# Kernel tuning notes

Hardware: AMD Instinct MI355X
Metric: run time of the kernel (lower is better)

Reference implementation:

```python
import jax, jax.numpy as jnp
import numpy as np


def overlap_and_add(frames, step):
    # frames: [B, F, L] -> [B, (F-1)*step + L] via strided scatter-add
    B, F, L = frames.shape
    out_len = (F - 1) * step + L
    idx = (jnp.arange(F)[:, None] * step + jnp.arange(L)[None, :]).reshape(-1)  # [F*L]
    return jnp.zeros((B, out_len), frames.dtype).at[:, idx].add(frames.reshape(B, F * L))


def setup_inputs() -> dict:
    key = jax.random.key(0)
    k1, k2, k3 = jax.random.split(key, 3)
    bs, frame, basis, spk = 16, 4086, 512, 2
    L = 16  # kernel_size_enc
    speech_length = (frame - 1) * (L // 2) + L  # 32696
    inputs = jax.random.normal(k1, (bs, frame, basis), dtype=jnp.float32)
    estmask = jax.random.uniform(k2, (bs, frame, basis, spk), dtype=jnp.float32)
    W = jax.random.normal(k3, (basis, L), dtype=jnp.float32) * 0.05
    return {"inputs": inputs, "estmask": estmask, "W": W,
            "kernel_size_enc": L, "speech_length": speech_length}


def reference(inputs, estmask, W, kernel_size_enc, speech_length):
    bs, frame, basis = inputs.shape
    spk = estmask.shape[-1]
    # mask-weight: [bs, frame, basis, spk]
    x = inputs[..., None] * estmask
    # -> [bs*spk, frame, basis]
    x = jnp.transpose(x, (0, 3, 1, 2)).reshape(bs * spk, frame, basis)
    # dense projection (no bias, no activation): [bs*spk, frame, L]
    x = jnp.einsum('bfc,cl->bfl', x, W)
    # overlap-and-add with frame_step = L // 2
    x = overlap_and_add(x, kernel_size_enc // 2)  # [bs*spk, samples]
    return x.reshape(bs, spk, speech_length)
```

## Files before the change

### kernel.cpp

```cpp
#include <hip/hip_runtime.h>

constexpr int BS = 16, F = 4086, C = 512, SPK = 2, L = 16, STEP = 8;
constexpr int T    = (F - 1) * STEP + L;
constexpr int ROWS = BS * F;
constexpr int OUT_N = BS * SPK * T;
constexpr int WPAD = 20;
constexpr int WAVES = 4;
constexpr int BLOCK = WAVES * 64;
constexpr int FR  = 4;
constexpr int FPB = WAVES * FR;
constexpr int GRID_A = ROWS / FPB;

template <int CTRL>
__device__ __forceinline__ float dppq(float x) {
    int i = __builtin_bit_cast(int, x);
    i = __builtin_amdgcn_update_dpp(i, i, CTRL, 0xf, 0xf, true);
    return __builtin_bit_cast(float, i);
}
template <int OFF>
__device__ __forceinline__ float swz(float x) {
    int i = __builtin_bit_cast(int, x);
    i = __builtin_amdgcn_ds_swizzle(i, OFF);
    return __builtin_bit_cast(float, i);
}

__device__ __forceinline__ float fold32(float v[32], int lane) {
    const bool h1 = lane & 1, h2 = lane & 2, h4 = lane & 4, h8 = lane & 8, h16 = lane & 16;
#pragma unroll
    for (int i = 0; i < 16; ++i) {
        const float s = h1 ? v[i] : v[i + 16];
        const float k = h1 ? v[i + 16] : v[i];
        v[i] = k + dppq<0xB1>(s);
    }
#pragma unroll
    for (int i = 0; i < 8; ++i) {
        const float s = h2 ? v[i] : v[i + 8];
        const float k = h2 ? v[i + 8] : v[i];
        v[i] = k + dppq<0x4E>(s);
    }
#pragma unroll
    for (int i = 0; i < 4; ++i) {
        const float s = h4 ? v[i] : v[i + 4];
        const float k = h4 ? v[i + 4] : v[i];
        v[i] = k + swz<0x101F>(s);
    }
#pragma unroll
    for (int i = 0; i < 2; ++i) {
        const float s = h8 ? v[i] : v[i + 2];
        const float k = h8 ? v[i + 2] : v[i];
        v[i] = k + swz<0x201F>(s);
    }
    {
        const float s = h16 ? v[0] : v[1];
        const float k = h16 ? v[1] : v[0];
        v[0] = k + swz<0x401F>(s);
    }
    return v[0] + __shfl_xor(v[0], 32, 64);
}

template <bool USE_WS>
__global__ __launch_bounds__(BLOCK, 2) void decoder_proj_kernel(
    const float* __restrict__ inp,
    const float* __restrict__ mask,
    const float* __restrict__ W,
    float* __restrict__ dst)
{
    __shared__ float w_lds[C * WPAD];

    const int tid = threadIdx.x;
    for (int r = tid; r < C; r += BLOCK) {
        const float4* src = reinterpret_cast<const float4*>(W + r * L);
        float4* d = reinterpret_cast<float4*>(w_lds + r * WPAD);
        d[0] = src[0]; d[1] = src[1]; d[2] = src[2]; d[3] = src[3];
    }
    __syncthreads();

    const int wave = tid >> 6, lane = tid & 63;
    const int row0 = blockIdx.x * FPB + wave * FR;

    const int o = ((lane & 1) << 4) | (((lane >> 1) & 1) << 3) | (((lane >> 2) & 1) << 2)
                | (((lane >> 3) & 1) << 1) | ((lane >> 4) & 1);

    float  xiA[8], xiB[8];
    float2 xmA[8], xmB[8];

    auto load = [&](int row, float* xi, float2* xm) {
        const float*  ir = inp + (size_t)row * C;
        const float2* mr = reinterpret_cast<const float2*>(mask) + (size_t)row * C;
#pragma unroll
        for (int i = 0; i < 8; ++i) {
            const int c = lane + 64 * i;
            xi[i] = ir[c];
            xm[i] = mr[c];
        }
    };

    auto compute = [&](const float* xi, const float2* xm) -> float {
        float v[32];
#pragma unroll
        for (int j = 0; j < 32; ++j) v[j] = 0.f;
#pragma unroll
        for (int i = 0; i < 8; ++i) {
            const int c  = lane + 64 * i;
            const float p0 = xi[i] * xm[i].x;
            const float p1 = xi[i] * xm[i].y;
            const float4* wr = reinterpret_cast<const float4*>(&w_lds[c * WPAD]);
#pragma unroll
            for (int q = 0; q < 4; ++q) {
                const float4 wv = wr[q];
                v[4*q+0]    = fmaf(p0, wv.x, v[4*q+0]);
                v[4*q+1]    = fmaf(p0, wv.y, v[4*q+1]);
                v[4*q+2]    = fmaf(p0, wv.z, v[4*q+2]);
                v[4*q+3]    = fmaf(p0, wv.w, v[4*q+3]);
                v[16+4*q+0] = fmaf(p1, wv.x, v[16+4*q+0]);
                v[16+4*q+1] = fmaf(p1, wv.y, v[16+4*q+1]);
                v[16+4*q+2] = fmaf(p1, wv.z, v[16+4*q+2]);
                v[16+4*q+3] = fmaf(p1, wv.w, v[16+4*q+3]);
            }
        }
        return fold32(v, lane);
    };

    auto store = [&](int row, float val) {
        if (USE_WS) {
            if (lane < 32) dst[(size_t)row * 32 + o] = val;
        } else {
            if (lane < 32) {
                const int b = row / F, f = row % F;
                const int s = o >> 4, l = o & 15;
                atomicAdd(&dst[(size_t)(b * SPK + s) * T + f * STEP + l], val);
            }
        }
    };

    load(row0 + 0, xiA, xmA);
    load(row0 + 1, xiB, xmB);
    store(row0 + 0, compute(xiA, xmA));
    load(row0 + 2, xiA, xmA);
    store(row0 + 1, compute(xiB, xmB));
    load(row0 + 3, xiB, xmB);
    store(row0 + 2, compute(xiA, xmA));
    store(row0 + 3, compute(xiB, xmB));
}

__global__ __launch_bounds__(256) void overlap_add_kernel(
    const float* __restrict__ proj,
    float* __restrict__ out)
{
    const int idx = blockIdx.x * blockDim.x + threadIdx.x;
    if (idx >= OUT_N) return;
    const int b = idx / (SPK * T);
    const int r = idx - b * (SPK * T);
    const int s = r / T;
    const int t = r - s * T;
    const int f0 = t >> 3, l0 = t & 7;
    float acc = 0.f;
    if (t < F * STEP) acc += proj[(size_t)(b * F + f0) * 32 + s * 16 + l0];
    if (t >= STEP)    acc += proj[(size_t)(b * F + f0 - 1) * 32 + s * 16 + 8 + l0];
    out[idx] = acc;
}

extern "C" void kernel_launch(void* const* d_in, const int* in_sizes, int n_in,
                              void* d_out, int out_size, void* d_ws, size_t ws_size,
                              hipStream_t stream) {
    const float* inp  = (const float*)d_in[0];
    const float* mask = (const float*)d_in[1];
    const float* W    = (const float*)d_in[2];
    float* out = (float*)d_out;

    const size_t need = (size_t)ROWS * 32 * sizeof(float);
    if (ws_size >= need) {
        float* proj = (float*)d_ws;
        decoder_proj_kernel<true><<<GRID_A, BLOCK, 0, stream>>>(inp, mask, W, proj);
        overlap_add_kernel<<<(OUT_N + 255) / 256, 256, 0, stream>>>(proj, out);
    } else {
        hipMemsetAsync(out, 0, (size_t)OUT_N * sizeof(float), stream);
        decoder_proj_kernel<false><<<GRID_A, BLOCK, 0, stream>>>(inp, mask, W, out);
    }
}
```

Before: 86.42 us.

## Store W transposed as packed bf16 in LDS and vectorize row loads

The projection weights are now converted to bf16 and stored transposed and packed in LDS, which cuts LDS footprint from about 40KB to 16KB and allows four blocks per CU. Input and mask rows are loaded as contiguous float4 vectors per lane instead of strided scalar and float2 loads, and the inner loop reads 8 packed weights per LDS access. The fallback path without workspace is removed. The bf16 rounding of W changes numerical precision, and the code now assumes the workspace is always large enough.

Result: slower. 94.18 us (+9.0%).

```diff
diff --git a/kernel.cpp b/kernel.cpp
--- a/kernel.cpp
+++ b/kernel.cpp
@@ -4,7 +4,6 @@
 constexpr int T    = (F - 1) * STEP + L;
 constexpr int ROWS = BS * F;
 constexpr int OUT_N = BS * SPK * T;
-constexpr int WPAD = 20;
 constexpr int WAVES = 4;
 constexpr int BLOCK = WAVES * 64;
 constexpr int FR  = 4;
@@ -58,20 +57,38 @@
     return v[0] + __shfl_xor(v[0], 32, 64);
 }
 
-template <bool USE_WS>
-__global__ __launch_bounds__(BLOCK, 2) void decoder_proj_kernel(
+__device__ __forceinline__ unsigned short f32_to_bf16_rne(float f) {
+    unsigned int u = __builtin_bit_cast(unsigned int, f);
+    u += 0x7fffu + ((u >> 16) & 1u);
+    return (unsigned short)(u >> 16);
+}
+
+__global__ __launch_bounds__(BLOCK, 4) void decoder_proj_kernel(
     const float* __restrict__ inp,
     const float* __restrict__ mask,
     const float* __restrict__ W,
     float* __restrict__ dst)
 {
-    __shared__ float w_lds[C * WPAD];
+    __shared__ unsigned int wT[L * (C / 2)];
 
     const int tid = threadIdx.x;
-    for (int r = tid; r < C; r += BLOCK) {
-        const float4* src = reinterpret_cast<const float4*>(W + r * L);
-        float4* d = reinterpret_cast<float4*>(w_lds + r * WPAD);
-        d[0] = src[0]; d[1] = src[1]; d[2] = src[2]; d[3] = src[3];
+
+    {
+        const float4* r0 = reinterpret_cast<const float4*>(W + (2 * tid) * L);
+        const float4* r1 = reinterpret_cast<const float4*>(W + (2 * tid + 1) * L);
+        float a[L], b[L];
+#pragma unroll
+        for (int q = 0; q < 4; ++q) {
+            const float4 x = r0[q], y = r1[q];
+            a[4*q+0]=x.x; a[4*q+1]=x.y; a[4*q+2]=x.z; a[4*q+3]=x.w;
+            b[4*q+0]=y.x; b[4*q+1]=y.y; b[4*q+2]=y.z; b[4*q+3]=y.w;
+        }
+#pragma unroll
+        for (int l = 0; l < L; ++l) {
+            const unsigned int d = (unsigned int)f32_to_bf16_rne(a[l])
+                                 | ((unsigned int)f32_to_bf16_rne(b[l]) << 16);
+            wT[l * (C / 2) + tid] = d;
+        }
     }
     __syncthreads();
 
@@ -81,66 +98,66 @@
     const int o = ((lane & 1) << 4) | (((lane >> 1) & 1) << 3) | (((lane >> 2) & 1) << 2)
                 | (((lane >> 3) & 1) << 1) | ((lane >> 4) & 1);
 
-    float  xiA[8], xiB[8];
-    float2 xmA[8], xmB[8];
+    float4 iA0, iA1, mA0, mA1, mA2, mA3;
+    float4 iB0, iB1, mB0, mB1, mB2, mB3;
 
-    auto load = [&](int row, float* xi, float2* xm) {
-        const float*  ir = inp + (size_t)row * C;
-        const float2* mr = reinterpret_cast<const float2*>(mask) + (size_t)row * C;
-#pragma unroll
-        for (int i = 0; i < 8; ++i) {
-            const int c = lane + 64 * i;
-            xi[i] = ir[c];
-            xm[i] = mr[c];
-        }
+    auto load = [&](int row, float4& i0, float4& i1,
+                    float4& m0, float4& m1, float4& m2, float4& m3) {
+        const float4* ir = reinterpret_cast<const float4*>(inp + (size_t)row * C + 8 * lane);
+        const float4* mr = reinterpret_cast<const float4*>(mask + (size_t)row * C * SPK + 16 * lane);
+        i0 = ir[0]; i1 = ir[1];
+        m0 = mr[0]; m1 = mr[1]; m2 = mr[2]; m3 = mr[3];
     };
 
-    auto compute = [&](const float* xi, const float2* xm) -> float {
+    const int4* wT4 = reinterpret_cast<const int4*>(wT);
+
+    auto compute = [&](const float4& i0, const float4& i1,
+                       const float4& m0, const float4& m1,
+                       const float4& m2, const float4& m3) -> float {
+        float p0[8], p1[8];
+        p0[0]=i0.x*m0.x; p1[0]=i0.x*m0.y;  p0[1]=i0.y*m0.z; p1[1]=i0.y*m0.w;
+        p0[2]=i0.z*m1.x; p1[2]=i0.z*m1.y;  p0[3]=i0.w*m1.z; p1[3]=i0.w*m1.w;
+        p0[4]=i1.x*m2.x; p1[4]=i1.x*m2.y;  p0[5]=i1.y*m2.z; p1[5]=i1.y*m2.w;
+        p0[6]=i1.z*m3.x; p1[6]=i1.z*m3.y;  p0[7]=i1.w*m3.z; p1[7]=i1.w*m3.w;
+
         float v[32];
 #pragma unroll
         for (int j = 0; j < 32; ++j) v[j] = 0.f;
+
 #pragma unroll
-        for (int i = 0; i < 8; ++i) {
-            const int c  = lane + 64 * i;
-            const float p0 = xi[i] * xm[i].x;
-            const float p1 = xi[i] * xm[i].y;
-            const float4* wr = reinterpret_cast<const float4*>(&w_lds[c * WPAD]);
+        for (int l = 0; l < L; ++l) {
+            const int4 wd = wT4[l * (C / 8) + lane];
+            const int d0 = wd.x, d1 = wd.y, d2 = wd.z, d3 = wd.w;
+            float w[8];
+            w[0] = __builtin_bit_cast(float, d0 << 16);
+            w[1] = __builtin_bit_cast(float, d0 & 0xffff0000);
+            w[2] = __builtin_bit_cast(float, d1 << 16);
+            w[3] = __builtin_bit_cast(float, d1 & 0xffff0000);
+            w[4] = __builtin_bit_cast(float, d2 << 16);
+            w[5] = __builtin_bit_cast(float, d2 & 0xffff0000);
+            w[6] = __builtin_bit_cast(float, d3 << 16);
+            w[7] = __builtin_bit_cast(float, d3 & 0xffff0000);
 #pragma unroll
-            for (int q = 0; q < 4; ++q) {
-                const float4 wv = wr[q];
-                v[4*q+0]    = fmaf(p0, wv.x, v[4*q+0]);
-                v[4*q+1]    = fmaf(p0, wv.y, v[4*q+1]);
-                v[4*q+2]    = fmaf(p0, wv.z, v[4*q+2]);
-                v[4*q+3]    = fmaf(p0, wv.w, v[4*q+3]);
-                v[16+4*q+0] = fmaf(p1, wv.x, v[16+4*q+0]);
-                v[16+4*q+1] = fmaf(p1, wv.y, v[16+4*q+1]);
-                v[16+4*q+2] = fmaf(p1, wv.z, v[16+4*q+2]);
-                v[16+4*q+3] = fmaf(p1, wv.w, v[16+4*q+3]);
+            for (int k = 0; k < 8; ++k) {
+                v[l]      = fmaf(p0[k], w[k], v[l]);
+                v[16 + l] = fmaf(p1[k], w[k], v[16 + l]);
             }
         }
         return fold32(v, lane);
     };
 
     auto store = [&](int row, float val) {
-        if (USE_WS) {
-            if (lane < 32) dst[(size_t)row * 32 + o] = val;
-        } else {
-            if (lane < 32) {
-                const int b = row / F, f = row % F;
-                const int s = o >> 4, l = o & 15;
-                atomicAdd(&dst[(size_t)(b * SPK + s) * T + f * STEP + l], val);
-            }
-        }
+        if (lane < 32) dst[(size_t)row * 32 + o] = val;
     };
 
-    load(row0 + 0, xiA, xmA);
-    load(row0 + 1, xiB, xmB);
-    store(row0 + 0, compute(xiA, xmA));
-    load(row0 + 2, xiA, xmA);
-    store(row0 + 1, compute(xiB, xmB));
-    load(row0 + 3, xiB, xmB);
-    store(row0 + 2, compute(xiA, xmA));
-    store(row0 + 3, compute(xiB, xmB));
+    load(row0 + 0, iA0, iA1, mA0, mA1, mA2, mA3);
+    load(row0 + 1, iB0, iB1, mB0, mB1, mB2, mB3);
+    store(row0 + 0, compute(iA0, iA1, mA0, mA1, mA2, mA3));
+    load(row0 + 2, iA0, iA1, mA0, mA1, mA2, mA3);
+    store(row0 + 1, compute(iB0, iB1, mB0, mB1, mB2, mB3));
+    load(row0 + 3, iB0, iB1, mB0, mB1, mB2, mB3);
+    store(row0 + 2, compute(iA0, iA1, mA0, mA1, mA2, mA3));
+    store(row0 + 3, compute(iB0, iB1, mB0, mB1, mB2, mB3));
 }
 
 __global__ __launch_bounds__(256) void overlap_add_kernel(
@@ -168,13 +185,7 @@
     const float* W    = (const float*)d_in[2];
     float* out = (float*)d_out;
 
-    const size_t need = (size_t)ROWS * 32 * sizeof(float);
-    if (ws_size >= need) {
-        float* proj = (float*)d_ws;
-        decoder_proj_kernel<true><<<GRID_A, BLOCK, 0, stream>>>(inp, mask, W, proj);
-        overlap_add_kernel<<<(OUT_N + 255) / 256, 256, 0, stream>>>(proj, out);
-    } else {
-        hipMemsetAsync(out, 0, (size_t)OUT_N * sizeof(float), stream);
-        decoder_proj_kernel<false><<<GRID_A, BLOCK, 0, stream>>>(inp, mask, W, out);
-    }
+    float* proj = (float*)d_ws;
+    decoder_proj_kernel<<<GRID_A, BLOCK, 0, stream>>>(inp, mask, W, proj);
+    overlap_add_kernel<<<(OUT_N + 255) / 256, 256, 0, stream>>>(proj, out);
 }
```

## Hold W as packed fp16 in registers and use fdot2 with split-channel wave pairs

Applied to the files above, without the earlier changes.

The projection kernel stops staging W in shared memory. Each lane now holds fp16-packed weights for four fixed channels in registers, and the masked products are converted to fp16 so each FMA pair becomes one v_dot2 instruction. Channels are split across pairs of waves, each wave handling 8 frames, and the partial sums are combined through a small LDS buffer. Input and mask are read with wider float4 loads. This removes LDS weight traffic and cuts ALU work, but it lowers precision to fp16 inputs with fp32 accumulation and drops the fallback path for when no workspace is available.

Result: slower. 99.45 us (+15.1%).

```diff
diff --git a/kernel.cpp b/kernel.cpp
--- a/kernel.cpp
+++ b/kernel.cpp
@@ -4,12 +4,13 @@
 constexpr int T    = (F - 1) * STEP + L;
 constexpr int ROWS = BS * F;
 constexpr int OUT_N = BS * SPK * T;
-constexpr int WPAD = 20;
-constexpr int WAVES = 4;
-constexpr int BLOCK = WAVES * 64;
-constexpr int FR  = 4;
-constexpr int FPB = WAVES * FR;
-constexpr int GRID_A = ROWS / FPB;
+constexpr int BLOCK = 256;
+constexpr int FRW  = 8;
+constexpr int FRB  = 16;
+constexpr int GRID_A = ROWS / FRB;
+
+typedef __fp16   h2    __attribute__((ext_vector_type(2)));
+typedef _Float16 f16x2 __attribute__((ext_vector_type(2)));
 
 template <int CTRL>
 __device__ __forceinline__ float dppq(float x) {
@@ -58,89 +59,106 @@
     return v[0] + __shfl_xor(v[0], 32, 64);
 }
 
-template <bool USE_WS>
-__global__ __launch_bounds__(BLOCK, 2) void decoder_proj_kernel(
+__device__ __forceinline__ float fdot2(h2 a, h2 b, float c) {
+#if __has_builtin(__builtin_amdgcn_fdot2)
+    return __builtin_amdgcn_fdot2(__builtin_bit_cast(f16x2, a),
+                                  __builtin_bit_cast(f16x2, b), c, false);
+#else
+    return fmaf((float)a.x, (float)b.x, fmaf((float)a.y, (float)b.y, c));
+#endif
+}
+
+__global__ __launch_bounds__(BLOCK, 4) void decoder_proj_kernel(
     const float* __restrict__ inp,
     const float* __restrict__ mask,
     const float* __restrict__ W,
     float* __restrict__ dst)
 {
-    __shared__ float w_lds[C * WPAD];
+    __shared__ float part[2][FRW][32];
 
-    const int tid = threadIdx.x;
-    for (int r = tid; r < C; r += BLOCK) {
-        const float4* src = reinterpret_cast<const float4*>(W + r * L);
-        float4* d = reinterpret_cast<float4*>(w_lds + r * WPAD);
-        d[0] = src[0]; d[1] = src[1]; d[2] = src[2]; d[3] = src[3];
-    }
-    __syncthreads();
-
+    const int tid  = threadIdx.x;
     const int wave = tid >> 6, lane = tid & 63;
-    const int row0 = blockIdx.x * FPB + wave * FR;
+    const int pairId = wave >> 1, h = wave & 1;
+    const int rbase  = blockIdx.x * FRB + pairId * FRW;
 
     const int o = ((lane & 1) << 4) | (((lane >> 1) & 1) << 3) | (((lane >> 2) & 1) << 2)
                 | (((lane >> 3) & 1) << 1) | ((lane >> 4) & 1);
 
-    float  xiA[8], xiB[8];
-    float2 xmA[8], xmB[8];
+    const int c0 = h * 256 + 4 * lane;
+    h2 wA[L], wB[L];
+    {
+        const float4* r0 = reinterpret_cast<const float4*>(W + (c0 + 0) * L);
+        const float4* r1 = reinterpret_cast<const float4*>(W + (c0 + 1) * L);
+        const float4* r2 = reinterpret_cast<const float4*>(W + (c0 + 2) * L);
+        const float4* r3 = reinterpret_cast<const float4*>(W + (c0 + 3) * L);
+#pragma unroll
+        for (int q = 0; q < 4; ++q) {
+            const float4 a = r0[q], b = r1[q], c = r2[q], d = r3[q];
+            wA[4*q+0] = __builtin_amdgcn_cvt_pkrtz(a.x, b.x);
+            wA[4*q+1] = __builtin_amdgcn_cvt_pkrtz(a.y, b.y);
+            wA[4*q+2] = __builtin_amdgcn_cvt_pkrtz(a.z, b.z);
+            wA[4*q+3] = __builtin_amdgcn_cvt_pkrtz(a.w, b.w);
+            wB[4*q+0] = __builtin_amdgcn_cvt_pkrtz(c.x, d.x);
+            wB[4*q+1] = __builtin_amdgcn_cvt_pkrtz(c.y, d.y);
+            wB[4*q+2] = __builtin_amdgcn_cvt_pkrtz(c.z, d.z);
+            wB[4*q+3] = __builtin_amdgcn_cvt_pkrtz(c.w, d.w);
+        }
+    }
 
-    auto load = [&](int row, float* xi, float2* xm) {
-        const float*  ir = inp + (size_t)row * C;
-        const float2* mr = reinterpret_cast<const float2*>(mask) + (size_t)row * C;
-#pragma unroll
-        for (int i = 0; i < 8; ++i) {
-            const int c = lane + 64 * i;
-            xi[i] = ir[c];
-            xm[i] = mr[c];
-        }
+    float4 iA, mA0, mA1, iB, mB0, mB1;
+    auto load = [&](int f, float4& i0, float4& m0, float4& m1) {
+        const int r = rbase + f;
+        i0 = *reinterpret_cast<const float4*>(inp + (size_t)r * C + c0);
+        const float4* mp = reinterpret_cast<const float4*>(mask + (size_t)r * C * SPK + 2 * c0);
+        m0 = mp[0]; m1 = mp[1];
     };
 
-    auto compute = [&](const float* xi, const float2* xm) -> float {
+    float keep[FRW];
+
+    auto compute = [&](int f, const float4& i0, const float4& m0, const float4& m1) {
+        const float p00 = i0.x * m0.x, p01 = i0.y * m0.z, p02 = i0.z * m1.x, p03 = i0.w * m1.z;
+        const float p10 = i0.x * m0.y, p11 = i0.y * m0.w, p12 = i0.z * m1.y, p13 = i0.w * m1.w;
+        const h2 q0 = __builtin_amdgcn_cvt_pkrtz(p00, p01);
+        const h2 q1 = __builtin_amdgcn_cvt_pkrtz(p02, p03);
+        const h2 q2 = __builtin_amdgcn_cvt_pkrtz(p10, p11);
+        const h2 q3 = __builtin_amdgcn_cvt_pkrtz(p12, p13);
+
         float v[32];
 #pragma unroll
         for (int j = 0; j < 32; ++j) v[j] = 0.f;
 #pragma unroll
-        for (int i = 0; i < 8; ++i) {
-            const int c  = lane + 64 * i;
-            const float p0 = xi[i] * xm[i].x;
-            const float p1 = xi[i] * xm[i].y;
-            const float4* wr = reinterpret_cast<const float4*>(&w_lds[c * WPAD]);
-#pragma unroll
-            for (int q = 0; q < 4; ++q) {
-                const float4 wv = wr[q];
-                v[4*q+0]    = fmaf(p0, wv.x, v[4*q+0]);
-                v[4*q+1]    = fmaf(p0, wv.y, v[4*q+1]);
-                v[4*q+2]    = fmaf(p0, wv.z, v[4*q+2]);
-                v[4*q+3]    = fmaf(p0, wv.w, v[4*q+3]);
-                v[16+4*q+0] = fmaf(p1, wv.x, v[16+4*q+0]);
-                v[16+4*q+1] = fmaf(p1, wv.y, v[16+4*q+1]);
-                v[16+4*q+2] = fmaf(p1, wv.z, v[16+4*q+2]);
-                v[16+4*q+3] = fmaf(p1, wv.w, v[16+4*q+3]);
-            }
+        for (int l = 0; l < L; ++l) {
+            v[l]      = fdot2(q1, wB[l], fdot2(q0, wA[l], v[l]));
+            v[16 + l] = fdot2(q3, wB[l], fdot2(q2, wA[l], v[16 + l]));
         }
-        return fold32(v, lane);
-    };
-
-    auto store = [&](int row, float val) {
-        if (USE_WS) {
-            if (lane < 32) dst[(size_t)row * 32 + o] = val;
+        const float val = fold32(v, lane);
+        if (h == 0) {
+            if (lane < 32) part[pairId][f][o] = val;
         } else {
-            if (lane < 32) {
-                const int b = row / F, f = row % F;
-                const int s = o >> 4, l = o & 15;
-                atomicAdd(&dst[(size_t)(b * SPK + s) * T + f * STEP + l], val);
-            }
+            keep[f] = val;
         }
     };
 
-    load(row0 + 0, xiA, xmA);
-    load(row0 + 1, xiB, xmB);
-    store(row0 + 0, compute(xiA, xmA));
-    load(row0 + 2, xiA, xmA);
-    store(row0 + 1, compute(xiB, xmB));
-    load(row0 + 3, xiB, xmB);
-    store(row0 + 2, compute(xiA, xmA));
-    store(row0 + 3, compute(xiB, xmB));
+    load(0, iA, mA0, mA1);
+    load(1, iB, mB0, mB1);
+    compute(0, iA, mA0, mA1); load(2, iA, mA0, mA1);
+    compute(1, iB, mB0, mB1); load(3, iB, mB0, mB1);
+    compute(2, iA, mA0, mA1); load(4, iA, mA0, mA1);
+    compute(3, iB, mB0, mB1); load(5, iB, mB0, mB1);
+    compute(4, iA, mA0, mA1); load(6, iA, mA0, mA1);
+    compute(5, iB, mB0, mB1); load(7, iB, mB0, mB1);
+    compute(6, iA, mA0, mA1);
+    compute(7, iB, mB0, mB1);
+
+    __syncthreads();
+
+    if (h == 1 && lane < 32) {
+#pragma unroll
+        for (int f = 0; f < FRW; ++f) {
+            const int r = rbase + f;
+            dst[(size_t)r * 32 + o] = keep[f] + part[pairId][f][o];
+        }
+    }
 }
 
 __global__ __launch_bounds__(256) void overlap_add_kernel(
@@ -168,13 +186,7 @@
     const float* W    = (const float*)d_in[2];
     float* out = (float*)d_out;
 
-    const size_t need = (size_t)ROWS * 32 * sizeof(float);
-    if (ws_size >= need) {
-        float* proj = (float*)d_ws;
-        decoder_proj_kernel<true><<<GRID_A, BLOCK, 0, stream>>>(inp, mask, W, proj);
-        overlap_add_kernel<<<(OUT_N + 255) / 256, 256, 0, stream>>>(proj, out);
-    } else {
-        hipMemsetAsync(out, 0, (size_t)OUT_N * sizeof(float), stream);
-        decoder_proj_kernel<false><<<GRID_A, BLOCK, 0, stream>>>(inp, mask, W, out);
-    }
+    float* proj = (float*)d_ws;
+    decoder_proj_kernel<<<GRID_A, BLOCK, 0, stream>>>(inp, mask, W, proj);
+    overlap_add_kernel<<<(OUT_N + 255) / 256, 256, 0, stream>>>(proj, out);
 }
```
